# Kernel optimization log

Hardware: AMD Instinct MI355X
Metric: run time of the kernel (lower is better)

The kernel has to match this reference:

```python
import jax, jax.numpy as jnp
import numpy as np

N, E = 50000, 800000
IN_DIM, H0, H1, OUT_DIM = 64, 64, 64, 8
NUM_RELS, NUM_BASES = 16, 8


def setup_inputs() -> dict:
    key = jax.random.key(0)
    ks = jax.random.split(key, 20)
    features = jax.random.normal(ks[0], (N, IN_DIM), dtype=jnp.float32)
    etypes = jax.random.randint(ks[1], (E,), 0, NUM_RELS)
    src = jax.random.randint(ks[2], (E,), 0, N)
    dst = jax.random.randint(ks[3], (E,), 0, N)
    # degree normalization 1/in_degree(dst), as DGL stores in g.edata['norm']
    deg = jax.ops.segment_sum(jnp.ones((E,), jnp.float32), dst, num_segments=N)
    norm = (1.0 / jnp.maximum(deg, 1.0))[dst][:, None]  # [E,1]

    def glorot(k, shape):
        fan_in, fan_out = shape[-2], shape[-1]
        lim = jnp.sqrt(6.0 / (fan_in + fan_out)).astype(jnp.float32)
        return jax.random.uniform(k, shape, jnp.float32, -lim, lim)

    dims = [(IN_DIM, H0), (H0, H1), (H1, OUT_DIM)]
    inp = {"features": features, "norm": norm}
    for i, (di, do) in enumerate(dims):
        inp[f"basis{i}"] = glorot(ks[4 + 4 * i], (NUM_BASES, di, do))
        inp[f"comp{i}"] = glorot(ks[5 + 4 * i], (NUM_RELS, NUM_BASES))
        inp[f"loop{i}"] = glorot(ks[6 + 4 * i], (di, do))
        inp[f"bias{i}"] = jnp.zeros((do,), jnp.float32)
    inp["etypes"] = etypes
    inp["src"] = src
    inp["dst"] = dst
    return inp


def rel_graph_conv(h, basis, comp, loop_w, bias, etypes, src, dst, norm, act):
    # basis-decomposed relation weights: [R, din, dout]
    W = jnp.einsum('rb,bio->rio', comp, basis)
    # transform every node under every relation: [N, R, dout]
    h_trans = jnp.einsum('ni,rio->nro', h, W)
    # per-edge gather of (src node, edge relation), degree-normalized
    msg = h_trans[src, etypes] * norm  # [E, dout]
    agg = jax.ops.segment_sum(msg, dst, num_segments=h.shape[0])  # [N, dout]
    out = agg + h @ loop_w + bias  # self-loop + bias (DGL defaults)
    return act(out)


def reference(features, norm, basis0, comp0, loop0, bias0, basis1, comp1, loop1,
              bias1, basis2, comp2, loop2, bias2, etypes, src, dst):
    lrelu = lambda x: jax.nn.leaky_relu(x, negative_slope=0.01)
    h = rel_graph_conv(features, basis0, comp0, loop0, bias0, etypes, src, dst, norm, lrelu)
    h = rel_graph_conv(h, basis1, comp1, loop1, bias1, etypes, src, dst, norm, lrelu)
    h = rel_graph_conv(h, basis2, comp2, loop2, bias2, etypes, src, dst, norm, jax.nn.relu)
    return h
```

## Files before the change

kernel.cpp:

```cpp
#include <hip/hip_runtime.h>

#define NN 50000
#define NE 800000
#define CAP 64
#define KC 72
#define CSTR 16

typedef __bf16 bf16x8 __attribute__((ext_vector_type(8)));
typedef float f32x4 __attribute__((ext_vector_type(4)));
typedef float f32x2 __attribute__((ext_vector_type(2)));
typedef unsigned short ushort;
typedef unsigned int uint;

__device__ inline ushort f2bf(float x) {
  uint u = __builtin_bit_cast(uint, x);
  u += 0x7FFF + ((u >> 16) & 1);
  return (ushort)(u >> 16);
}
__device__ inline float bf2f(ushort u) {
  return __builtin_bit_cast(float, (uint)u << 16);
}


__device__ inline void wprep_body(const float* __restrict__ basis,
                                  const float* __restrict__ loopw,
                                  ushort* __restrict__ W2, int DOUT, int NCOLS,
                                  int idx) {
  int total = KC * NCOLS * 8;
  if (idx >= total) return;
  int j = idx & 7;
  int n = (idx >> 3) % NCOLS;
  int kc = idx / (8 * NCOLS);
  int k = kc * 8 + j;
  float v = 0.f;
  if (n < DOUT) v = (k < 512) ? basis[k * DOUT + n] : loopw[(k - 512) * DOUT + n];
  W2[((size_t)kc * NCOLS + n) * 8 + j] = f2bf(v);
}

__global__ __launch_bounds__(256) void build_kernel(
    const int* __restrict__ dstv, const int* __restrict__ srcv,
    const int* __restrict__ etv, int* __restrict__ cursor, int* __restrict__ pk,
    const float* __restrict__ f, ushort* __restrict__ fb,
    const float* __restrict__ b0, const float* __restrict__ l0, ushort* __restrict__ W0,
    const float* __restrict__ b1, const float* __restrict__ l1, ushort* __restrict__ W1,
    const float* __restrict__ b2, const float* __restrict__ l2, ushort* __restrict__ W2,
    const float* __restrict__ c0, const float* __restrict__ c1,
    const float* __restrict__ c2, float* __restrict__ cp) {
  int blk = blockIdx.x;
  int tid = threadIdx.x;
  if (blk < 3125) {
    int i = blk * 256 + tid;
    int d = dstv[i];
    int p = atomicAdd(&cursor[(size_t)d * CSTR], 1);
    if (p < CAP) pk[d * CAP + p] = (etv[i] << 16) | srcv[i];
  } else if (blk < 6250) {
    int i = (blk - 3125) * 256 + tid;
    float4 v = ((const float4*)f)[i];
    ushort4 u;
    u.x = f2bf(v.x); u.y = f2bf(v.y); u.z = f2bf(v.z); u.w = f2bf(v.w);
    ((ushort4*)fb)[i] = u;
  } else if (blk < 6394) {
    wprep_body(b0, l0, W0, 64, 64, (blk - 6250) * 256 + tid);
  } else if (blk < 6538) {
    wprep_body(b1, l1, W1, 64, 64, (blk - 6394) * 256 + tid);
  } else if (blk < 6574) {
    wprep_body(b2, l2, W2, 8, 16, (blk - 6538) * 256 + tid);
  } else {
    int idx = (blk - 6574) * 256 + tid;
    if (idx < 408) {
      int l = idx / 136, k = idx % 136;
      const float* src = (l == 0) ? c0 : ((l == 1) ? c1 : c2);
      cp[idx] = (k < 128) ? src[k] : 0.f;
    }
  }
}


template <int DOUT, int NCOLS, bool OBF>
__global__ __launch_bounds__(1024, 8) void layer_kernel(
    const ushort* __restrict__ hb,
    const float* __restrict__ cpad,
    const int* __restrict__ degv,
    const int* __restrict__ pk,
    const ushort* __restrict__ W2,
    const float* __restrict__ bias,
    void* __restrict__ outp,
    float slope)
{
  __shared__ ushort X[KC][16][8];
  int tid = threadIdx.x;
  int wave = tid >> 6;
  int lane = tid & 63;
  int dbase = blockIdx.x * 16;
  int d = __builtin_amdgcn_readfirstlane(dbase + wave);

  int deg = degv[(size_t)d * CSTR];
  int dw = deg > CAP ? CAP : deg;
  const int4* p4 = (const int4*)(pk + (size_t)d * CAP);

  f32x2 acc2[4] = {{0.f, 0.f}, {0.f, 0.f}, {0.f, 0.f}, {0.f, 0.f}};
  for (int base = 0; base < dw; base += 8) {
    int qg = base >> 3;
    int4 e0 = p4[qg * 2];
    int4 e1 = p4[qg * 2 + 1];
    int pe[8] = {e0.x, e0.y, e0.z, e0.w, e1.x, e1.y, e1.z, e1.w};
    float hv[8];
    int ps[8];
#pragma unroll
    for (int i = 0; i < 8; ++i) {
      int pr = __builtin_amdgcn_readfirstlane(pe[i]);
      ps[i] = (base + i < dw) ? pr : (16 << 16);
      hv[i] = bf2f(hb[(size_t)(ps[i] & 0xFFFF) * 64 + lane]);
    }
#pragma unroll
    for (int i = 0; i < 8; ++i) {
      const f32x2* c2 = (const f32x2*)(cpad + (ps[i] >> 16) * 8);
      f32x2 h2 = {hv[i], hv[i]};
#pragma unroll
      for (int j = 0; j < 4; ++j)
        acc2[j] = __builtin_elementwise_fma(c2[j], h2, acc2[j]);
    }
  }

  float inv = 1.0f / (float)(deg > 1 ? deg : 1);
  int jj = lane & 7;
  int csub = lane >> 3;
#pragma unroll
  for (int b = 0; b < 8; ++b) {
    float v = ((b & 1) ? acc2[b >> 1].y : acc2[b >> 1].x) * inv;
    X[b * 8 + csub][wave ^ csub][jj] = f2bf(v);
  }
  X[64 + csub][wave ^ csub][jj] = hb[(size_t)d * 64 + lane];
  __syncthreads();

  if (wave < (DOUT == 64 ? 4 : 1)) {
    int q = lane >> 4;
    int r = lane & 15;
    f32x4 accd = {0.f, 0.f, 0.f, 0.f};
#pragma unroll
    for (int ks = 0; ks < 18; ++ks) {
      int kc = ks * 4 + q;
      bf16x8 bfrag = *(const bf16x8*)&X[kc][r ^ (kc & 7)][0];
      bf16x8 afrag = *(const bf16x8*)(W2 + ((size_t)kc * NCOLS + wave * 16 + r) * 8);
      accd = __builtin_amdgcn_mfma_f32_16x16x32_bf16(afrag, bfrag, accd, 0, 0, 0);
    }
    int m = dbase + r;
    int nb = wave * 16 + q * 4;
    if (nb < DOUT) {
      float4 bv = *(const float4*)(bias + nb);
      float v0 = accd[0] + bv.x;
      float v1 = accd[1] + bv.y;
      float v2 = accd[2] + bv.z;
      float v3 = accd[3] + bv.w;
      v0 = v0 > 0.f ? v0 : slope * v0;
      v1 = v1 > 0.f ? v1 : slope * v1;
      v2 = v2 > 0.f ? v2 : slope * v2;
      v3 = v3 > 0.f ? v3 : slope * v3;
      if (OBF) {
        ushort4 u;
        u.x = f2bf(v0); u.y = f2bf(v1); u.z = f2bf(v2); u.w = f2bf(v3);
        *(ushort4*)((ushort*)outp + (size_t)m * DOUT + nb) = u;
      } else {
        *(float4*)((float*)outp + (size_t)m * DOUT + nb) = float4{v0, v1, v2, v3};
      }
    }
  }
}


extern "C" void kernel_launch(void* const* d_in, const int* in_sizes, int n_in,
                              void* d_out, int out_size, void* d_ws, size_t ws_size,
                              hipStream_t stream) {
  const float* features = (const float*)d_in[0];
  const float* basis0   = (const float*)d_in[2];
  const float* comp0    = (const float*)d_in[3];
  const float* loop0    = (const float*)d_in[4];
  const float* bias0    = (const float*)d_in[5];
  const float* basis1   = (const float*)d_in[6];
  const float* comp1    = (const float*)d_in[7];
  const float* loop1    = (const float*)d_in[8];
  const float* bias1    = (const float*)d_in[9];
  const float* basis2   = (const float*)d_in[10];
  const float* comp2    = (const float*)d_in[11];
  const float* loop2    = (const float*)d_in[12];
  const float* bias2    = (const float*)d_in[13];
  const int* etypes     = (const int*)d_in[14];
  const int* srcv       = (const int*)d_in[15];
  const int* dstv       = (const int*)d_in[16];

  char* ws = (char*)d_ws;
  size_t off = 0;
  auto alloc = [&](size_t bytes) {
    void* p = ws + off;
    off += (bytes + 255) & ~(size_t)255;
    return p;
  };
  int* cnt      = (int*)alloc((size_t)NN * CSTR * sizeof(int));
  int* pk       = (int*)alloc((size_t)NN * CAP * sizeof(int));
  ushort* W2_0  = (ushort*)alloc((size_t)KC * 64 * 8 * sizeof(ushort));
  ushort* W2_1  = (ushort*)alloc((size_t)KC * 64 * 8 * sizeof(ushort));
  ushort* W2_2  = (ushort*)alloc((size_t)KC * 16 * 8 * sizeof(ushort));
  float* cpad   = (float*)alloc(3 * 136 * sizeof(float));
  ushort* fbf   = (ushort*)alloc((size_t)NN * 64 * sizeof(ushort));
  ushort* hA    = (ushort*)alloc((size_t)NN * 64 * sizeof(ushort));
  ushort* hB    = (ushort*)alloc((size_t)NN * 64 * sizeof(ushort));

  hipMemsetAsync(cnt, 0, (size_t)NN * CSTR * sizeof(int), stream);
  build_kernel<<<6576, 256, 0, stream>>>(dstv, srcv, etypes, cnt, pk,
                                         features, fbf,
                                         basis0, loop0, W2_0,
                                         basis1, loop1, W2_1,
                                         basis2, loop2, W2_2,
                                         comp0, comp1, comp2, cpad);

  layer_kernel<64, 64, true><<<3125, 1024, 0, stream>>>(
      fbf, cpad + 0 * 136, cnt, pk, W2_0, bias0, hA, 0.01f);
  layer_kernel<64, 64, true><<<3125, 1024, 0, stream>>>(
      hA, cpad + 1 * 136, cnt, pk, W2_1, bias1, hB, 0.01f);
  layer_kernel<8, 16, false><<<3125, 1024, 0, stream>>>(
      hB, cpad + 2 * 136, cnt, pk, W2_2, bias2, d_out, 0.0f);
}
```

Baseline: 175.9 us.

## Use 8-node blocks, 16-edge gather batches, dense counters, and paired edge inserts

Several changes land together. The degree counters are packed densely instead of padded to 16-int stride. The build kernel handles two edges per thread. The pk array is memset to 0xFF so padding entries can be clamped branchlessly (relation capped at 16, src capped at NN-1) instead of compared against degree. The layer kernel now uses 512-thread blocks covering 8 destination nodes and gathers 16 neighbor rows per batch to raise memory-level parallelism. The cost is half-empty MFMA tiles (only 8 of 16 rows are used), an extra 12.8MB memset, and more same-line atomic contention on the dense counters.

```diff
diff --git a/kernel.cpp b/kernel.cpp
--- a/kernel.cpp
+++ b/kernel.cpp
@@ -4,11 +4,9 @@
 #define NE 800000
 #define CAP 64
 #define KC 72
-#define CSTR 16
 
 typedef __bf16 bf16x8 __attribute__((ext_vector_type(8)));
 typedef float f32x4 __attribute__((ext_vector_type(4)));
-typedef float f32x2 __attribute__((ext_vector_type(2)));
 typedef unsigned short ushort;
 typedef unsigned int uint;
 
@@ -48,25 +46,32 @@
     const float* __restrict__ c2, float* __restrict__ cp) {
   int blk = blockIdx.x;
   int tid = threadIdx.x;
-  if (blk < 3125) {
+  if (blk < 1563) {
     int i = blk * 256 + tid;
-    int d = dstv[i];
-    int p = atomicAdd(&cursor[(size_t)d * CSTR], 1);
-    if (p < CAP) pk[d * CAP + p] = (etv[i] << 16) | srcv[i];
-  } else if (blk < 6250) {
-    int i = (blk - 3125) * 256 + tid;
+    if (i < NE / 2) {
+      int j1 = i + NE / 2;
+      int d0 = dstv[i], d1 = dstv[j1];
+      int s0 = srcv[i], s1 = srcv[j1];
+      int e0 = etv[i], e1 = etv[j1];
+      int p0 = atomicAdd(&cursor[d0], 1);
+      int p1 = atomicAdd(&cursor[d1], 1);
+      if (p0 < CAP) pk[d0 * CAP + p0] = (e0 << 16) | s0;
+      if (p1 < CAP) pk[d1 * CAP + p1] = (e1 << 16) | s1;
+    }
+  } else if (blk < 4688) {
+    int i = (blk - 1563) * 256 + tid;
     float4 v = ((const float4*)f)[i];
     ushort4 u;
     u.x = f2bf(v.x); u.y = f2bf(v.y); u.z = f2bf(v.z); u.w = f2bf(v.w);
     ((ushort4*)fb)[i] = u;
-  } else if (blk < 6394) {
-    wprep_body(b0, l0, W0, 64, 64, (blk - 6250) * 256 + tid);
-  } else if (blk < 6538) {
-    wprep_body(b1, l1, W1, 64, 64, (blk - 6394) * 256 + tid);
-  } else if (blk < 6574) {
-    wprep_body(b2, l2, W2, 8, 16, (blk - 6538) * 256 + tid);
+  } else if (blk < 4832) {
+    wprep_body(b0, l0, W0, 64, 64, (blk - 4688) * 256 + tid);
+  } else if (blk < 4976) {
+    wprep_body(b1, l1, W1, 64, 64, (blk - 4832) * 256 + tid);
+  } else if (blk < 5012) {
+    wprep_body(b2, l2, W2, 8, 16, (blk - 4976) * 256 + tid);
   } else {
-    int idx = (blk - 6574) * 256 + tid;
+    int idx = (blk - 5012) * 256 + tid;
     if (idx < 408) {
       int l = idx / 136, k = idx % 136;
       const float* src = (l == 0) ? c0 : ((l == 1) ? c1 : c2);
@@ -77,7 +82,7 @@
 
 
 template <int DOUT, int NCOLS, bool OBF>
-__global__ __launch_bounds__(1024, 8) void layer_kernel(
+__global__ __launch_bounds__(512, 4) void layer_kernel(
     const ushort* __restrict__ hb,
     const float* __restrict__ cpad,
     const int* __restrict__ degv,
@@ -91,34 +96,39 @@
   int tid = threadIdx.x;
   int wave = tid >> 6;
   int lane = tid & 63;
-  int dbase = blockIdx.x * 16;
+  int dbase = blockIdx.x * 8;
   int d = __builtin_amdgcn_readfirstlane(dbase + wave);
 
-  int deg = degv[(size_t)d * CSTR];
+  int deg = degv[d];
   int dw = deg > CAP ? CAP : deg;
   const int4* p4 = (const int4*)(pk + (size_t)d * CAP);
 
-  f32x2 acc2[4] = {{0.f, 0.f}, {0.f, 0.f}, {0.f, 0.f}, {0.f, 0.f}};
-  for (int base = 0; base < dw; base += 8) {
-    int qg = base >> 3;
-    int4 e0 = p4[qg * 2];
-    int4 e1 = p4[qg * 2 + 1];
-    int pe[8] = {e0.x, e0.y, e0.z, e0.w, e1.x, e1.y, e1.z, e1.w};
-    float hv[8];
-    int ps[8];
-#pragma unroll
-    for (int i = 0; i < 8; ++i) {
-      int pr = __builtin_amdgcn_readfirstlane(pe[i]);
-      ps[i] = (base + i < dw) ? pr : (16 << 16);
-      hv[i] = bf2f(hb[(size_t)(ps[i] & 0xFFFF) * 64 + lane]);
-    }
-#pragma unroll
-    for (int i = 0; i < 8; ++i) {
-      const f32x2* c2 = (const f32x2*)(cpad + (ps[i] >> 16) * 8);
-      f32x2 h2 = {hv[i], hv[i]};
-#pragma unroll
-      for (int j = 0; j < 4; ++j)
-        acc2[j] = __builtin_elementwise_fma(c2[j], h2, acc2[j]);
+  float acc[8] = {0.f, 0.f, 0.f, 0.f, 0.f, 0.f, 0.f, 0.f};
+  for (int base = 0; base < dw; base += 16) {
+    int4 g0 = p4[(base >> 2) + 0];
+    int4 g1 = p4[(base >> 2) + 1];
+    int4 g2 = p4[(base >> 2) + 2];
+    int4 g3 = p4[(base >> 2) + 3];
+    int pe[16] = {g0.x, g0.y, g0.z, g0.w, g1.x, g1.y, g1.z, g1.w,
+                  g2.x, g2.y, g2.z, g2.w, g3.x, g3.y, g3.z, g3.w};
+    uint rs[16], ss[16];
+#pragma unroll
+    for (int i = 0; i < 16; ++i) {
+      uint up = (uint)__builtin_amdgcn_readfirstlane(pe[i]);
+      uint r = up >> 16;
+      rs[i] = r > 16u ? 16u : r;
+      uint s = up & 0xFFFFu;
+      ss[i] = s > (uint)(NN - 1) ? (uint)(NN - 1) : s;
+    }
+    ushort hu[16];
+#pragma unroll
+    for (int i = 0; i < 16; ++i) hu[i] = hb[(size_t)ss[i] * 64 + lane];
+#pragma unroll
+    for (int i = 0; i < 16; ++i) {
+      float hv = bf2f(hu[i]);
+      const float* c = cpad + rs[i] * 8;
+#pragma unroll
+      for (int b = 0; b < 8; ++b) acc[b] = fmaf(c[b], hv, acc[b]);
     }
   }
 
@@ -126,10 +136,8 @@
   int jj = lane & 7;
   int csub = lane >> 3;
 #pragma unroll
-  for (int b = 0; b < 8; ++b) {
-    float v = ((b & 1) ? acc2[b >> 1].y : acc2[b >> 1].x) * inv;
-    X[b * 8 + csub][wave ^ csub][jj] = f2bf(v);
-  }
+  for (int b = 0; b < 8; ++b)
+    X[b * 8 + csub][wave ^ csub][jj] = f2bf(acc[b] * inv);
   X[64 + csub][wave ^ csub][jj] = hb[(size_t)d * 64 + lane];
   __syncthreads();
 
@@ -146,7 +154,7 @@
     }
     int m = dbase + r;
     int nb = wave * 16 + q * 4;
-    if (nb < DOUT) {
+    if (r < 8 && nb < DOUT) {
       float4 bv = *(const float4*)(bias + nb);
       float v0 = accd[0] + bv.x;
       float v1 = accd[1] + bv.y;
@@ -195,7 +203,7 @@
     off += (bytes + 255) & ~(size_t)255;
     return p;
   };
-  int* cnt      = (int*)alloc((size_t)NN * CSTR * sizeof(int));
+  int* cnt      = (int*)alloc(NN * sizeof(int));
   int* pk       = (int*)alloc((size_t)NN * CAP * sizeof(int));
   ushort* W2_0  = (ushort*)alloc((size_t)KC * 64 * 8 * sizeof(ushort));
   ushort* W2_1  = (ushort*)alloc((size_t)KC * 64 * 8 * sizeof(ushort));
@@ -205,18 +213,19 @@
   ushort* hA    = (ushort*)alloc((size_t)NN * 64 * sizeof(ushort));
   ushort* hB    = (ushort*)alloc((size_t)NN * 64 * sizeof(ushort));
 
-  hipMemsetAsync(cnt, 0, (size_t)NN * CSTR * sizeof(int), stream);
-  build_kernel<<<6576, 256, 0, stream>>>(dstv, srcv, etypes, cnt, pk,
+  hipMemsetAsync(cnt, 0, NN * sizeof(int), stream);
+  hipMemsetAsync(pk, 0xFF, (size_t)NN * CAP * sizeof(int), stream);
+  build_kernel<<<5014, 256, 0, stream>>>(dstv, srcv, etypes, cnt, pk,
                                          features, fbf,
                                          basis0, loop0, W2_0,
                                          basis1, loop1, W2_1,
                                          basis2, loop2, W2_2,
                                          comp0, comp1, comp2, cpad);
 
-  layer_kernel<64, 64, true><<<3125, 1024, 0, stream>>>(
+  layer_kernel<64, 64, true><<<6250, 512, 0, stream>>>(
       fbf, cpad + 0 * 136, cnt, pk, W2_0, bias0, hA, 0.01f);
-  layer_kernel<64, 64, true><<<3125, 1024, 0, stream>>>(
+  layer_kernel<64, 64, true><<<6250, 512, 0, stream>>>(
       hA, cpad + 1 * 136, cnt, pk, W2_1, bias1, hB, 0.01f);
-  layer_kernel<8, 16, false><<<3125, 1024, 0, stream>>>(
+  layer_kernel<8, 16, false><<<6250, 512, 0, stream>>>(
       hB, cpad + 2 * 136, cnt, pk, W2_2, bias2, d_out, 0.0f);
 }
```

After: 204.7 us. 1.16x slower.
